# Optimization experiments

Hardware: AMD Instinct MI355X
Metric: run time of the kernel (lower is better)

Reference implementation:

```python
import jax, jax.numpy as jnp
import numpy as np

EPS_BN = 1e-5   # torch BatchNorm1d default eps
EPS_W = 1e-8    # inverse-distance weighting eps


def linear_bn_relu(x, W, b, gamma, beta, mean, var):
    # x: [B, N, Cin]; W: [Cout, Cin]. BatchNorm applied in eval mode with running stats.
    y = jnp.einsum('bnc,oc->bno', x, W) + b
    y = (y - mean) * (gamma / jnp.sqrt(var + EPS_BN)) + beta
    return jax.nn.relu(y)


def interpolate3(xyz_tgt, xyz_src, feats_src):
    # 3-NN inverse-distance-weighted interpolation (PointNetFeaturePropagation, mlp=[]).
    # xyz_tgt: [B,N,3], xyz_src: [B,S,3], feats_src: [B,S,C] -> [B,N,C]
    d = (jnp.sum(xyz_tgt * xyz_tgt, -1, keepdims=True)
         - 2.0 * jnp.einsum('bnd,bsd->bns', xyz_tgt, xyz_src)
         + jnp.sum(xyz_src * xyz_src, -1)[:, None, :])       # [B,N,S] squared dists
    neg_d, idx = jax.lax.top_k(-d, 3)                          # 3 smallest distances
    dists = -neg_d                                             # [B,N,3]
    w = 1.0 / (dists + EPS_W)
    w = w / jnp.sum(w, -1, keepdims=True)                      # [B,N,3]
    gathered = jax.vmap(lambda f, i: f[i])(feats_src, idx)     # [B,N,3,C]
    return jnp.sum(gathered * w[..., None], axis=2)            # [B,N,C]


def setup_inputs() -> dict:
    key = jax.random.key(0)
    ks = jax.random.split(key, 16)
    B, N1, N2 = 4, 4096, 16384
    dim1, dim2, dim_out = 512, 256, 256
    inp = {
        'xyz1': jax.random.normal(ks[0], (B, N1, 3), jnp.float32),
        'points1': jax.random.normal(ks[1], (B, N1, dim1), jnp.float32),
        'xyz2': jax.random.normal(ks[2], (B, N2, 3), jnp.float32),
        'points2': jax.random.normal(ks[3], (B, N2, dim2), jnp.float32),
        # fc1: Linear(dim1, dim_out) + BN(dim_out)
        'W1': jax.random.normal(ks[4], (dim_out, dim1), jnp.float32) * (dim1 ** -0.5),
        'b1': jax.random.normal(ks[5], (dim_out,), jnp.float32) * 0.01,
        'g1': jax.random.uniform(ks[6], (dim_out,), jnp.float32, 0.5, 1.5),
        'be1': jax.random.normal(ks[7], (dim_out,), jnp.float32) * 0.01,
        'm1': jax.random.normal(ks[8], (dim_out,), jnp.float32) * 0.01,
        'v1': jax.random.uniform(ks[9], (dim_out,), jnp.float32, 0.5, 1.5),
        # fc2: Linear(dim2, dim_out) + BN(dim_out)
        'W2': jax.random.normal(ks[10], (dim_out, dim2), jnp.float32) * (dim2 ** -0.5),
        'b2': jax.random.normal(ks[11], (dim_out,), jnp.float32) * 0.01,
        'g2': jax.random.uniform(ks[12], (dim_out,), jnp.float32, 0.5, 1.5),
        'be2': jax.random.normal(ks[13], (dim_out,), jnp.float32) * 0.01,
        'm2': jax.random.normal(ks[14], (dim_out,), jnp.float32) * 0.01,
        'v2': jax.random.uniform(ks[15], (dim_out,), jnp.float32, 0.5, 1.5),
    }
    return inp


def reference(xyz1, points1, xyz2, points2,
              W1, b1, g1, be1, m1, v1,
              W2, b2, g2, be2, m2, v2):
    feats1 = linear_bn_relu(points1, W1, b1, g1, be1, m1, v1)  # [B,N1,dim_out]
    feats2 = linear_bn_relu(points2, W2, b2, g2, be2, m2, v2)  # [B,N2,dim_out]
    interp = interpolate3(xyz2, xyz1, feats1)                  # [B,N2,dim_out]
    return interp + feats2
```

## Files before the change

kernel.cpp:

```cpp
#include <hip/hip_runtime.h>
#include <math.h>

#define EPS_BN 1e-5f

typedef __attribute__((ext_vector_type(8))) short bf16x8;
typedef __attribute__((ext_vector_type(4))) float f32x4;
typedef __attribute__((ext_vector_type(8))) _Float16 fp16x8;
typedef __attribute__((ext_vector_type(16))) float f32x16;

__device__ __forceinline__ void gld_lds16(const void* g, void* l) {
    __builtin_amdgcn_global_load_lds(
        (const __attribute__((address_space(1))) unsigned int*)g,
        (__attribute__((address_space(3))) unsigned int*)l, 16, 0, 0);
}

__device__ __forceinline__ unsigned short f2bf(float f) {
    unsigned u = __float_as_uint(f);
    return (unsigned short)((u + 0x7FFFu + ((u >> 16) & 1u)) >> 16);
}

__device__ __forceinline__ float dist_exact(float4 T, float4 s) {
    float dot2 = __fadd_rn(__fadd_rn(__fmul_rn(T.x, s.x), __fmul_rn(T.y, s.y)),
                           __fmul_rn(T.z, s.z));
    return __fadd_rn(__fsub_rn(T.w, dot2), s.w);
}

__device__ __forceinline__ float min3f(float a, float b, float c) {
    float d;
    asm("v_min3_f32 %0, %1, %2, %3" : "=v"(d) : "v"(a), "v"(b), "v"(c));
    return d;
}
__device__ __forceinline__ unsigned med3u(unsigned a, unsigned b, unsigned c) {
    unsigned d;
    asm("v_med3_u32 %0, %1, %2, %3" : "=v"(d) : "v"(a), "v"(b), "v"(c));
    return d;
}

__device__ __forceinline__ void conv_body(
    const float* __restrict__ src, unsigned short* __restrict__ dst,
    int blk, int tid, int K8log, int nslab)
{
    const int gid = blk * 256 + tid;
    const int m  = gid >> K8log;
    const int ko = gid & ((1 << K8log) - 1);
    const float4* s = (const float4*)src + ((size_t)m << (K8log + 1)) + ko * 2;
    float4 f0 = s[0];
    float4 f1 = s[1];
    const int mblk = m >> 7, r = m & 127;
    const int slab = ko >> 2, o = ko & 3;
    const int g = (o + (r >> 1)) & 3;
    unsigned short h[8] = {f2bf(f0.x), f2bf(f0.y), f2bf(f0.z), f2bf(f0.w),
                           f2bf(f1.x), f2bf(f1.y), f2bf(f1.z), f2bf(f1.w)};
    *(uint4*)(dst + ((size_t)(mblk * nslab + slab)) * 4096 + r * 32 + g * 8) =
        *(uint4*)h;
}

__global__ __launch_bounds__(256) void prep_all(
    const float* __restrict__ p1, const float* __restrict__ p2,
    const float* __restrict__ w1, const float* __restrict__ w2,
    unsigned short* __restrict__ A1p, unsigned short* __restrict__ A2p,
    unsigned short* __restrict__ W1p, unsigned short* __restrict__ W2p,
    const float* __restrict__ xyz1, const float* __restrict__ xyz2,
    float4* __restrict__ sxyz1, _Float16* __restrict__ srcpk,
    _Float16* __restrict__ tgtpk, float4* __restrict__ txyz2)
{
    const int blk = blockIdx.x, tid = threadIdx.x;
    if (blk < 4096)        conv_body(p1, A1p, blk,         tid, 6, 16);
    else if (blk < 12288)  conv_body(p2, A2p, blk - 4096,  tid, 5, 8);
    else if (blk < 12352)  conv_body(w1, W1p, blk - 12288, tid, 6, 16);
    else if (blk < 12384)  conv_body(w2, W2p, blk - 12352, tid, 5, 8);
    else if (blk < 12448) {
        int i = (blk - 12384) * 256 + tid;
        float x = xyz1[i * 3 + 0], y = xyz1[i * 3 + 1], z = xyz1[i * 3 + 2];
        float ss = __fadd_rn(__fadd_rn(__fmul_rn(x, x), __fmul_rn(y, y)),
                             __fmul_rn(z, z));
        float x2 = x + x, y2 = y + y, z2 = z + z;
        sxyz1[i] = make_float4(x2, y2, z2, ss);
        float nx = -x2, ny = -y2, nz = -z2;
        _Float16 hx = (_Float16)nx, lx = (_Float16)(nx - (float)hx);
        _Float16 hy = (_Float16)ny, ly = (_Float16)(ny - (float)hy);
        _Float16 hz = (_Float16)nz, lz = (_Float16)(nz - (float)hz);
        _Float16 hw = (_Float16)ss, lw = (_Float16)(ss - (float)hw);
        _Float16 z0 = (_Float16)0.f;
        fp16x8 lo8 = {hx, hx, lx, hy, hy, ly, hz, hz};
        fp16x8 hi8 = {lz, hw, lw, z0, z0, z0, z0, z0};
        *(fp16x8*)(srcpk + (size_t)i * 16)     = lo8;
        *(fp16x8*)(srcpk + (size_t)i * 16 + 8) = hi8;
    } else {
        int i = (blk - 12448) * 256 + tid;
        float x = xyz2[i * 3 + 0], y = xyz2[i * 3 + 1], z = xyz2[i * 3 + 2];
        float st = __fadd_rn(__fadd_rn(__fmul_rn(x, x), __fmul_rn(y, y)),
                             __fmul_rn(z, z));
        txyz2[i] = make_float4(x, y, z, st);
        _Float16 hx = (_Float16)x, lx = (_Float16)(x - (float)hx);
        _Float16 hy = (_Float16)y, ly = (_Float16)(y - (float)hy);
        _Float16 hz = (_Float16)z, lz = (_Float16)(z - (float)hz);
        _Float16 z0 = (_Float16)0.f, one = (_Float16)1.0f;
        fp16x8 lo8 = {hx, lx, hx, hy, ly, hy, hz, lz};
        fp16x8 hi8 = {hz, one, one, z0, z0, z0, z0, z0};
        *(fp16x8*)(tgtpk + (size_t)i * 16)     = lo8;
        *(fp16x8*)(tgtpk + (size_t)i * 16 + 8) = hi8;
    }
}

__global__ __launch_bounds__(256) void knn_mfma(
    const float4* __restrict__ sxyz1,
    const _Float16* __restrict__ srcpk,
    const _Float16* __restrict__ tgtpk,
    const float4* __restrict__ txyz2,
    float* __restrict__ w3, int* __restrict__ idx3)
{
    const int tid  = threadIdx.x;
    const int wv   = tid >> 6;
    const int lane = tid & 63;
    const int col  = lane & 31;
    const int h    = lane >> 5;
    const int tgt  = blockIdx.x * 128 + wv * 32 + col;
    const int batch = tgt >> 14;

    const float4 T = txyz2[tgt];
    const fp16x8 bfrag = *(const fp16x8*)(tgtpk + (size_t)tgt * 16 + h * 8);
    const _Float16* __restrict__ ap =
        srcpk + (size_t)batch * 4096 * 16 + (size_t)col * 16 + h * 8;
    const float4* __restrict__ S = sxyz1 + batch * 4096;

    const f32x16 zacc = {0.f,0.f,0.f,0.f, 0.f,0.f,0.f,0.f,
                         0.f,0.f,0.f,0.f, 0.f,0.f,0.f,0.f};

    unsigned k0 = 0xFFFFFFFFu, k1 = 0xFFFFFFFFu, k2 = 0xFFFFFFFFu,
             k3 = 0xFFFFFFFFu, k4 = 0xFFFFFFFFu, k5 = 0xFFFFFFFFu,
             k6 = 0xFFFFFFFFu, k7 = 0xFFFFFFFFu, k8 = 0xFFFFFFFFu,
             k9 = 0xFFFFFFFFu, k10 = 0xFFFFFFFFu, k11 = 0xFFFFFFFFu;

#pragma unroll 4
    for (int b = 0; b < 128; b++) {
        fp16x8 afrag = *(const fp16x8*)(ap + (size_t)b * 512);
        f32x16 acc = __builtin_amdgcn_mfma_f32_32x32x16_f16(
            afrag, bfrag, zacc, 0, 0, 0);
        float m1 = min3f(acc[0], acc[1], acc[2]);
        float m2 = min3f(acc[3], acc[4], acc[5]);
        float m3 = min3f(acc[6], acc[7], acc[8]);
        float m4 = min3f(acc[9], acc[10], acc[11]);
        float m5 = min3f(acc[12], acc[13], acc[14]);
        float m6 = min3f(m1, m2, m3);
        float m7 = min3f(m4, m5, acc[15]);
        float m  = fminf(m6, m7);

        int fu = __float_as_int(m);
        unsigned fk = (unsigned)(fu ^ ((fu >> 31) | 0x80000000));
        unsigned key = (fk & 0xFFFFFF80u) | (unsigned)b;

        unsigned nk0 = key < k0 ? key : k0;
        k11 = med3u(key, k10, k11);
        k10 = med3u(key, k9, k10);
        k9  = med3u(key, k8, k9);
        k8  = med3u(key, k7, k8);
        k7  = med3u(key, k6, k7);
        k6  = med3u(key, k5, k6);
        k5  = med3u(key, k4, k5);
        k4  = med3u(key, k3, k4);
        k3  = med3u(key, k2, k3);
        k2  = med3u(key, k1, k2);
        k1  = med3u(key, k0, k1);
        k0  = nk0;
    }

    const double INITK = __hiloint2double(0x7F800000, 0);
    double K0 = INITK, K1 = INITK, K2 = INITK;
#define INS3(kk) { if ((kk) < K2) {                                  \
        if ((kk) < K1) { K2 = K1;                                    \
            if ((kk) < K0) { K1 = K0; K0 = (kk); } else K1 = (kk);   \
        } else K2 = (kk); } }

#pragma unroll 1
    for (int r = 0; r < 12; r++) {
        const int bb = (int)(k0 & 127u);
        const float4* Sb = S + bb * 32 + 4 * h;
        const int sbase = bb * 32 + 4 * h;
#pragma unroll
        for (int e = 0; e < 16; e++) {
            const int row = (e & 3) + 8 * (e >> 2);
            float4 s = Sb[row];
            float d = dist_exact(T, s);
            double kk = __hiloint2double(__float_as_int(d), sbase + row);
            INS3(kk);
        }
        k0 = k1; k1 = k2; k2 = k3; k3 = k4; k4 = k5; k5 = k6;
        k6 = k7; k7 = k8; k8 = k9; k9 = k10; k10 = k11;
    }

    double O0 = __shfl_xor(K0, 32);
    double O1 = __shfl_xor(K1, 32);
    double O2 = __shfl_xor(K2, 32);
    INS3(O0); INS3(O1); INS3(O2);
#undef INS3

    if (h == 0) {
        float d0 = __int_as_float(__double2hiint(K0));
        float d1 = __int_as_float(__double2hiint(K1));
        float d2 = __int_as_float(__double2hiint(K2));
        float w0 = 1.0f / __fadd_rn(d0, 1e-8f);
        float w1 = 1.0f / __fadd_rn(d1, 1e-8f);
        float w2 = 1.0f / __fadd_rn(d2, 1e-8f);
        float ws = __fadd_rn(__fadd_rn(w0, w1), w2);
        w3[(size_t)tgt * 3 + 0] = w0 / ws;
        w3[(size_t)tgt * 3 + 1] = w1 / ws;
        w3[(size_t)tgt * 3 + 2] = w2 / ws;
        idx3[(size_t)tgt * 3 + 0] = __double2loint(K0);
        idx3[(size_t)tgt * 3 + 1] = __double2loint(K1);
        idx3[(size_t)tgt * 3 + 2] = __double2loint(K2);
    }
}

__global__ __launch_bounds__(256) void gemm_bf16_bn_relu(
    const unsigned short* __restrict__ Ap,
    const unsigned short* __restrict__ Bp,
    const float* __restrict__ bias,
    const float* __restrict__ gamma,
    const float* __restrict__ beta,
    const float* __restrict__ mean,
    const float* __restrict__ var,
    float* __restrict__ out, int M, int K)
{
    __shared__ __align__(16) unsigned short As[4096];
    __shared__ __align__(16) unsigned short Bs[4096];

    const int tid  = threadIdx.x;
    const int w    = tid >> 6;
    const int lane = tid & 63;
    const int q    = lane >> 4;
    const int rl   = lane & 15;
    const int wm   = w >> 1, wn = w & 1;
    const int bn   = blockIdx.x, bm = blockIdx.y;
    const int nslab = K >> 5;

    f32x4 acc[4][4];
#pragma unroll
    for (int i = 0; i < 4; i++)
#pragma unroll
        for (int j = 0; j < 4; j++) acc[i][j] = (f32x4){0.f, 0.f, 0.f, 0.f};

    const unsigned short* Ab = Ap + (size_t)bm * nslab * 4096;
    const unsigned short* Bb = Bp + (size_t)bn * nslab * 4096;
    const int c0 = 2 * w;
    const int l8 = lane * 8;

    int aidx[4], bidx[4];
#pragma unroll
    for (int i = 0; i < 4; i++) {
        int rr = wm * 64 + i * 16 + rl;
        aidx[i] = rr * 32 + ((q + (rr >> 1)) & 3) * 8;
        int nn = wn * 64 + i * 16 + rl;
        bidx[i] = nn * 32 + ((q + (nn >> 1)) & 3) * 8;
    }

    for (int s = 0; s < nslab; s++) {
        __syncthreads();
        const unsigned short* a = Ab + (size_t)s * 4096;
        const unsigned short* b = Bb + (size_t)s * 4096;
        gld_lds16(a + (c0 + 0) * 512 + l8, &As[(c0 + 0) * 512 + l8]);
        gld_lds16(a + (c0 + 1) * 512 + l8, &As[(c0 + 1) * 512 + l8]);
        gld_lds16(b + (c0 + 0) * 512 + l8, &Bs[(c0 + 0) * 512 + l8]);
        gld_lds16(b + (c0 + 1) * 512 + l8, &Bs[(c0 + 1) * 512 + l8]);
        __syncthreads();

        bf16x8 af[4], bf[4];
#pragma unroll
        for (int i = 0; i < 4; i++) af[i] = *(const bf16x8*)&As[aidx[i]];
#pragma unroll
        for (int j = 0; j < 4; j++) bf[j] = *(const bf16x8*)&Bs[bidx[j]];
#pragma unroll
        for (int i = 0; i < 4; i++)
#pragma unroll
            for (int j = 0; j < 4; j++)
                acc[i][j] = __builtin_amdgcn_mfma_f32_16x16x32_bf16(
                    af[i], bf[j], acc[i][j], 0, 0, 0);
    }

    const int gm0 = bm * 128 + wm * 64;
    const int gn0 = bn * 128 + wn * 64;
#pragma unroll
    for (int j = 0; j < 4; j++) {
        int n = gn0 + j * 16 + rl;
        float sc = gamma[n] / sqrtf(var[n] + EPS_BN);
        float sh = beta[n] + (bias[n] - mean[n]) * sc;
#pragma unroll
        for (int i = 0; i < 4; i++) {
            int m0 = gm0 + i * 16 + q * 4;
#pragma unroll
            for (int t = 0; t < 4; t++) {
                float v = fmaxf(acc[i][j][t] * sc + sh, 0.f);
                out[(size_t)(m0 + t) * 256 + n] = v;
            }
        }
    }
}

__global__ __launch_bounds__(256) void gemm2_interp(
    const unsigned short* __restrict__ Ap,
    const unsigned short* __restrict__ Bp,
    const float* __restrict__ bias,
    const float* __restrict__ gamma,
    const float* __restrict__ beta,
    const float* __restrict__ mean,
    const float* __restrict__ var,
    const float* __restrict__ feats1,
    const float* __restrict__ w3,
    const int*   __restrict__ idx3,
    float* __restrict__ out)
{
    __shared__ __align__(16) unsigned short As[4096];
    __shared__ __align__(16) unsigned short Bs[4096];

    const int tid  = threadIdx.x;
    const int w    = tid >> 6;
    const int lane = tid & 63;
    const int q    = lane >> 4;
    const int rl   = lane & 15;
    const int wm   = w >> 1, wn = w & 1;
    const int bn   = blockIdx.x, bm = blockIdx.y;
    const int nslab = 8;

    f32x4 acc[4][4];
#pragma unroll
    for (int i = 0; i < 4; i++)
#pragma unroll
        for (int j = 0; j < 4; j++) acc[i][j] = (f32x4){0.f, 0.f, 0.f, 0.f};

    const unsigned short* Ab = Ap + (size_t)bm * nslab * 4096;
    const unsigned short* Bb = Bp + (size_t)bn * nslab * 4096;
    const int c0 = 2 * w;
    const int l8 = lane * 8;

    int aidx[4], bidx[4];
#pragma unroll
    for (int i = 0; i < 4; i++) {
        int rr = wm * 64 + i * 16 + rl;
        aidx[i] = rr * 32 + ((q + (rr >> 1)) & 3) * 8;
        int nn = wn * 64 + i * 16 + rl;
        bidx[i] = nn * 32 + ((q + (nn >> 1)) & 3) * 8;
    }

    for (int s = 0; s < nslab; s++) {
        __syncthreads();
        const unsigned short* a = Ab + (size_t)s * 4096;
        const unsigned short* b = Bb + (size_t)s * 4096;
        gld_lds16(a + (c0 + 0) * 512 + l8, &As[(c0 + 0) * 512 + l8]);
        gld_lds16(a + (c0 + 1) * 512 + l8, &As[(c0 + 1) * 512 + l8]);
        gld_lds16(b + (c0 + 0) * 512 + l8, &Bs[(c0 + 0) * 512 + l8]);
        gld_lds16(b + (c0 + 1) * 512 + l8, &Bs[(c0 + 1) * 512 + l8]);
        __syncthreads();

        bf16x8 af[4], bf[4];
#pragma unroll
        for (int i = 0; i < 4; i++) af[i] = *(const bf16x8*)&As[aidx[i]];
#pragma unroll
        for (int j = 0; j < 4; j++) bf[j] = *(const bf16x8*)&Bs[bidx[j]];
#pragma unroll
        for (int i = 0; i < 4; i++)
#pragma unroll
            for (int j = 0; j < 4; j++)
                acc[i][j] = __builtin_amdgcn_mfma_f32_16x16x32_bf16(
                    af[i], bf[j], acc[i][j], 0, 0, 0);
    }

    const int gm0 = bm * 128 + wm * 64;
    const int gn0 = bn * 128 + wn * 64;
    float scj[4], shj[4];
    int nj[4];
#pragma unroll
    for (int j = 0; j < 4; j++) {
        int n = gn0 + j * 16 + rl;
        nj[j] = n;
        float sc = gamma[n] / sqrtf(var[n] + EPS_BN);
        scj[j] = sc;
        shj[j] = beta[n] + (bias[n] - mean[n]) * sc;
    }

#pragma unroll
    for (int i = 0; i < 4; i++) {
#pragma unroll
        for (int t = 0; t < 4; t++) {
            const int m = gm0 + i * 16 + q * 4 + t;
            const int bb = m >> 14;
            const int j0 = idx3[(size_t)m * 3 + 0];
            const int j1 = idx3[(size_t)m * 3 + 1];
            const int j2 = idx3[(size_t)m * 3 + 2];
            const float u0 = w3[(size_t)m * 3 + 0];
            const float u1 = w3[(size_t)m * 3 + 1];
            const float u2 = w3[(size_t)m * 3 + 2];
            const float* f0 = feats1 + ((size_t)(bb * 4096 + j0)) * 256;
            const float* f1 = feats1 + ((size_t)(bb * 4096 + j1)) * 256;
            const float* f2 = feats1 + ((size_t)(bb * 4096 + j2)) * 256;
#pragma unroll
            for (int j = 0; j < 4; j++) {
                const int n = nj[j];
                float v = fmaxf(acc[i][j][t] * scj[j] + shj[j], 0.f);
                v += u0 * f0[n] + u1 * f1[n] + u2 * f2[n];
                out[(size_t)m * 256 + n] = v;
            }
        }
    }
}

extern "C" void kernel_launch(void* const* d_in, const int* in_sizes, int n_in,
                              void* d_out, int out_size, void* d_ws, size_t ws_size,
                              hipStream_t stream) {
    const float* xyz1    = (const float*)d_in[0];
    const float* points1 = (const float*)d_in[1];
    const float* xyz2    = (const float*)d_in[2];
    const float* points2 = (const float*)d_in[3];
    const float* W1  = (const float*)d_in[4];
    const float* b1  = (const float*)d_in[5];
    const float* g1  = (const float*)d_in[6];
    const float* be1 = (const float*)d_in[7];
    const float* m1  = (const float*)d_in[8];
    const float* v1  = (const float*)d_in[9];
    const float* W2  = (const float*)d_in[10];
    const float* b2  = (const float*)d_in[11];
    const float* g2  = (const float*)d_in[12];
    const float* be2 = (const float*)d_in[13];
    const float* m2  = (const float*)d_in[14];
    const float* v2  = (const float*)d_in[15];

    const size_t MB = 1u << 20;
    char* ws = (char*)d_ws;
    float*          feats1 = (float*)(ws);
    _Float16*       srcpk  = (_Float16*)(ws);
    _Float16*       tgtpk  = (_Float16*)(ws + 1 * MB);
    unsigned short* A1p    = (unsigned short*)(ws + 16 * MB);
    unsigned short* A2p    = (unsigned short*)(ws + 32 * MB);
    unsigned short* W1p    = (unsigned short*)(ws + 64 * MB);
    unsigned short* W2p    = (unsigned short*)(ws + 64 * MB + 512 * 1024);
    float4*         sxyz1  = (float4*)(ws + 65 * MB);
    float4*         txyz2  = (float4*)(ws + 66 * MB);
    float*          w3     = (float*)(ws + 67 * MB);
    int*            idx3   = (int*)(ws + 68 * MB);
    float* outp = (float*)d_out;

    dim3 blk(256);
    prep_all<<<12704, blk, 0, stream>>>(points1, points2, W1, W2,
                                        A1p, A2p, W1p, W2p,
                                        xyz1, xyz2, sxyz1, srcpk, tgtpk, txyz2);
    knn_mfma<<<512, blk, 0, stream>>>(sxyz1, srcpk, tgtpk, txyz2, w3, idx3);
    gemm_bf16_bn_relu<<<dim3(2, 128), blk, 0, stream>>>(A1p, W1p, b1, g1, be1, m1, v1,
                                                        feats1, 16384, 512);
    gemm2_interp<<<dim3(2, 512), blk, 0, stream>>>(A2p, W2p, b2, g2, be2, m2, v2,
                                                   feats1, w3, idx3, outp);
}
```

Before: 317.3 us.

## Split KNN source scan into four partitions with a separate merge kernel

The KNN kernel now splits the 4096 source points of each batch into four partitions of 32 MFMA tiles each. It launches four times as many blocks, and each block writes its partial top-3 candidates (packed distance and index) to a workspace buffer. A new merge kernel reduces the 12 candidates per target and computes the inverse-distance weights. The A-fragment load is also software-prefetched one iteration ahead. This raises occupancy and parallelism on a grid that previously had only 512 blocks, at the cost of repeating the 12-round exact-distance refinement per partition, an extra kernel launch, and extra global traffic for the candidates.

```diff
diff --git a/kernel.cpp b/kernel.cpp
--- a/kernel.cpp
+++ b/kernel.cpp
@@ -103,25 +103,27 @@
     }
 }
 
-__global__ __launch_bounds__(256) void knn_mfma(
+__global__ __launch_bounds__(256) void knn_part(
     const float4* __restrict__ sxyz1,
     const _Float16* __restrict__ srcpk,
     const _Float16* __restrict__ tgtpk,
     const float4* __restrict__ txyz2,
-    float* __restrict__ w3, int* __restrict__ idx3)
+    double* __restrict__ cand)
 {
     const int tid  = threadIdx.x;
     const int wv   = tid >> 6;
     const int lane = tid & 63;
     const int col  = lane & 31;
     const int h    = lane >> 5;
-    const int tgt  = blockIdx.x * 128 + wv * 32 + col;
+    const int grp  = blockIdx.x & 511;
+    const int part = blockIdx.x >> 9;
+    const int tgt  = grp * 128 + wv * 32 + col;
     const int batch = tgt >> 14;
 
     const float4 T = txyz2[tgt];
     const fp16x8 bfrag = *(const fp16x8*)(tgtpk + (size_t)tgt * 16 + h * 8);
     const _Float16* __restrict__ ap =
-        srcpk + (size_t)batch * 4096 * 16 + (size_t)col * 16 + h * 8;
+        srcpk + (size_t)batch * 65536 + (size_t)col * 16 + h * 8;
     const float4* __restrict__ S = sxyz1 + batch * 4096;
 
     const f32x16 zacc = {0.f,0.f,0.f,0.f, 0.f,0.f,0.f,0.f,
@@ -132,11 +134,14 @@
              k6 = 0xFFFFFFFFu, k7 = 0xFFFFFFFFu, k8 = 0xFFFFFFFFu,
              k9 = 0xFFFFFFFFu, k10 = 0xFFFFFFFFu, k11 = 0xFFFFFFFFu;
 
+    const int b0 = part * 32;
+    fp16x8 af = *(const fp16x8*)(ap + (size_t)b0 * 512);
 #pragma unroll 4
-    for (int b = 0; b < 128; b++) {
-        fp16x8 afrag = *(const fp16x8*)(ap + (size_t)b * 512);
+    for (int b = b0; b < b0 + 32; b++) {
+        fp16x8 afn = af;
+        if (b < b0 + 31) afn = *(const fp16x8*)(ap + (size_t)(b + 1) * 512);
         f32x16 acc = __builtin_amdgcn_mfma_f32_32x32x16_f16(
-            afrag, bfrag, zacc, 0, 0, 0);
+            af, bfrag, zacc, 0, 0, 0);
         float m1 = min3f(acc[0], acc[1], acc[2]);
         float m2 = min3f(acc[3], acc[4], acc[5]);
         float m3 = min3f(acc[6], acc[7], acc[8]);
@@ -163,6 +168,7 @@
         k2  = med3u(key, k1, k2);
         k1  = med3u(key, k0, k1);
         k0  = nk0;
+        af = afn;
     }
 
     const double INITK = __hiloint2double(0x7F800000, 0);
@@ -196,20 +202,42 @@
 #undef INS3
 
     if (h == 0) {
-        float d0 = __int_as_float(__double2hiint(K0));
-        float d1 = __int_as_float(__double2hiint(K1));
-        float d2 = __int_as_float(__double2hiint(K2));
-        float w0 = 1.0f / __fadd_rn(d0, 1e-8f);
-        float w1 = 1.0f / __fadd_rn(d1, 1e-8f);
-        float w2 = 1.0f / __fadd_rn(d2, 1e-8f);
-        float ws = __fadd_rn(__fadd_rn(w0, w1), w2);
-        w3[(size_t)tgt * 3 + 0] = w0 / ws;
-        w3[(size_t)tgt * 3 + 1] = w1 / ws;
-        w3[(size_t)tgt * 3 + 2] = w2 / ws;
-        idx3[(size_t)tgt * 3 + 0] = __double2loint(K0);
-        idx3[(size_t)tgt * 3 + 1] = __double2loint(K1);
-        idx3[(size_t)tgt * 3 + 2] = __double2loint(K2);
-    }
+        double* c = cand + (size_t)tgt * 12 + part * 3;
+        c[0] = K0; c[1] = K1; c[2] = K2;
+    }
+}
+
+__global__ __launch_bounds__(256) void knn_merge(
+    const double* __restrict__ cand, float* __restrict__ w3,
+    int* __restrict__ idx3)
+{
+    const int g = blockIdx.x * 256 + threadIdx.x;
+    const double INIT = __hiloint2double(0x7F800000, 0);
+    double k0 = INIT, k1 = INIT, k2 = INIT;
+#pragma unroll
+    for (int p = 0; p < 12; p++) {
+        double k = cand[(size_t)g * 12 + p];
+        if (k < k2) {
+            if (k < k1) {
+                k2 = k1;
+                if (k < k0) { k1 = k0; k0 = k; }
+                else        { k1 = k; }
+            } else { k2 = k; }
+        }
+    }
+    float d0 = __int_as_float(__double2hiint(k0));
+    float d1 = __int_as_float(__double2hiint(k1));
+    float d2 = __int_as_float(__double2hiint(k2));
+    float w0 = 1.0f / __fadd_rn(d0, 1e-8f);
+    float w1 = 1.0f / __fadd_rn(d1, 1e-8f);
+    float w2 = 1.0f / __fadd_rn(d2, 1e-8f);
+    float ws = __fadd_rn(__fadd_rn(w0, w1), w2);
+    w3[(size_t)g * 3 + 0] = w0 / ws;
+    w3[(size_t)g * 3 + 1] = w1 / ws;
+    w3[(size_t)g * 3 + 2] = w2 / ws;
+    idx3[(size_t)g * 3 + 0] = __double2loint(k0);
+    idx3[(size_t)g * 3 + 1] = __double2loint(k1);
+    idx3[(size_t)g * 3 + 2] = __double2loint(k2);
 }
 
 __global__ __launch_bounds__(256) void gemm_bf16_bn_relu(
@@ -428,6 +456,7 @@
     float*          feats1 = (float*)(ws);
     _Float16*       srcpk  = (_Float16*)(ws);
     _Float16*       tgtpk  = (_Float16*)(ws + 1 * MB);
+    double*         cand   = (double*)(ws + 4 * MB);
     unsigned short* A1p    = (unsigned short*)(ws + 16 * MB);
     unsigned short* A2p    = (unsigned short*)(ws + 32 * MB);
     unsigned short* W1p    = (unsigned short*)(ws + 64 * MB);
@@ -442,7 +471,8 @@
     prep_all<<<12704, blk, 0, stream>>>(points1, points2, W1, W2,
                                         A1p, A2p, W1p, W2p,
                                         xyz1, xyz2, sxyz1, srcpk, tgtpk, txyz2);
-    knn_mfma<<<512, blk, 0, stream>>>(sxyz1, srcpk, tgtpk, txyz2, w3, idx3);
+    knn_part<<<2048, blk, 0, stream>>>(sxyz1, srcpk, tgtpk, txyz2, cand);
+    knn_merge<<<256, blk, 0, stream>>>(cand, w3, idx3);
     gemm_bf16_bn_relu<<<dim3(2, 128), blk, 0, stream>>>(A1p, W1p, b1, g1, be1, m1, v1,
                                                         feats1, 16384, 512);
     gemm2_interp<<<dim3(2, 512), blk, 0, stream>>>(A2p, W2p, b2, g2, be2, m2, v2,
```

Measured after the change: 406.2 us. +28.0%, slower.

## Split KNN source scan across four waves per target group with LDS merge

Applied to the files above, without the earlier changes.

The KNN kernel now has each block handle 32 targets instead of 128. Its four waves each scan a quarter of the 128 source blocks. The per-wave top-12 block keys are merged through LDS, each wave refines three of the merged candidates exactly, and a final LDS reduction picks the top three. This shortens the serial 128-step chain per thread and launches four times as many blocks, adding a software prefetch of the next A fragment. The cost is two barriers, an extra 48-key insertion pass, and more LDS use per block.

```diff
diff --git a/kernel.cpp b/kernel.cpp
--- a/kernel.cpp
+++ b/kernel.cpp
@@ -103,25 +103,29 @@
     }
 }
 
-__global__ __launch_bounds__(256) void knn_mfma(
+__global__ __launch_bounds__(256) void knn_fused(
     const float4* __restrict__ sxyz1,
     const _Float16* __restrict__ srcpk,
     const _Float16* __restrict__ tgtpk,
     const float4* __restrict__ txyz2,
     float* __restrict__ w3, int* __restrict__ idx3)
 {
+    __shared__ unsigned keys_lds[64 * 49];
+    __shared__ double   tails_lds[32 * 13];
+
     const int tid  = threadIdx.x;
     const int wv   = tid >> 6;
     const int lane = tid & 63;
     const int col  = lane & 31;
     const int h    = lane >> 5;
-    const int tgt  = blockIdx.x * 128 + wv * 32 + col;
+    const int tgtg = blockIdx.x;
+    const int tgt  = tgtg * 32 + col;
     const int batch = tgt >> 14;
 
     const float4 T = txyz2[tgt];
     const fp16x8 bfrag = *(const fp16x8*)(tgtpk + (size_t)tgt * 16 + h * 8);
     const _Float16* __restrict__ ap =
-        srcpk + (size_t)batch * 4096 * 16 + (size_t)col * 16 + h * 8;
+        srcpk + (size_t)batch * 65536 + (size_t)col * 16 + h * 8;
     const float4* __restrict__ S = sxyz1 + batch * 4096;
 
     const f32x16 zacc = {0.f,0.f,0.f,0.f, 0.f,0.f,0.f,0.f,
@@ -132,11 +136,14 @@
              k6 = 0xFFFFFFFFu, k7 = 0xFFFFFFFFu, k8 = 0xFFFFFFFFu,
              k9 = 0xFFFFFFFFu, k10 = 0xFFFFFFFFu, k11 = 0xFFFFFFFFu;
 
+    const int b0 = wv * 32;
+    fp16x8 af = *(const fp16x8*)(ap + (size_t)b0 * 512);
 #pragma unroll 4
-    for (int b = 0; b < 128; b++) {
-        fp16x8 afrag = *(const fp16x8*)(ap + (size_t)b * 512);
+    for (int b = b0; b < b0 + 32; b++) {
+        fp16x8 afn = af;
+        if (b < b0 + 31) afn = *(const fp16x8*)(ap + (size_t)(b + 1) * 512);
         f32x16 acc = __builtin_amdgcn_mfma_f32_32x32x16_f16(
-            afrag, bfrag, zacc, 0, 0, 0);
+            af, bfrag, zacc, 0, 0, 0);
         float m1 = min3f(acc[0], acc[1], acc[2]);
         float m2 = min3f(acc[3], acc[4], acc[5]);
         float m3 = min3f(acc[6], acc[7], acc[8]);
@@ -163,7 +170,50 @@
         k2  = med3u(key, k1, k2);
         k1  = med3u(key, k0, k1);
         k0  = nk0;
-    }
+        af = afn;
+    }
+
+    {
+        unsigned* kw = &keys_lds[(h * 32 + col) * 49 + wv * 12];
+        kw[0] = k0;  kw[1] = k1;  kw[2] = k2;  kw[3] = k3;
+        kw[4] = k4;  kw[5] = k5;  kw[6] = k6;  kw[7] = k7;
+        kw[8] = k8;  kw[9] = k9;  kw[10] = k10; kw[11] = k11;
+    }
+    __syncthreads();
+
+    unsigned s0 = 0xFFFFFFFFu, s1 = 0xFFFFFFFFu, s2 = 0xFFFFFFFFu,
+             s3 = 0xFFFFFFFFu, s4 = 0xFFFFFFFFu, s5 = 0xFFFFFFFFu,
+             s6 = 0xFFFFFFFFu, s7 = 0xFFFFFFFFu, s8 = 0xFFFFFFFFu,
+             s9 = 0xFFFFFFFFu, s10 = 0xFFFFFFFFu, s11 = 0xFFFFFFFFu;
+#define INSK(key) {                                                   \
+        unsigned n0 = (key) < s0 ? (key) : s0;                        \
+        s11 = med3u((key), s10, s11);                                 \
+        s10 = med3u((key), s9, s10);                                  \
+        s9  = med3u((key), s8, s9);                                   \
+        s8  = med3u((key), s7, s8);                                   \
+        s7  = med3u((key), s6, s7);                                   \
+        s6  = med3u((key), s5, s6);                                   \
+        s5  = med3u((key), s4, s5);                                   \
+        s4  = med3u((key), s3, s4);                                   \
+        s3  = med3u((key), s2, s3);                                   \
+        s2  = med3u((key), s1, s2);                                   \
+        s1  = med3u((key), s0, s1);                                   \
+        s0  = n0; }
+    {
+        const unsigned* kr = &keys_lds[(h * 32 + col) * 49];
+#pragma unroll 8
+        for (int c = 0; c < 48; c++) {
+            unsigned key = kr[c];
+            INSK(key);
+        }
+    }
+#undef INSK
+
+    unsigned r0, r1, r2;
+    if      (wv == 0) { r0 = s0; r1 = s1;  r2 = s2;  }
+    else if (wv == 1) { r0 = s3; r1 = s4;  r2 = s5;  }
+    else if (wv == 2) { r0 = s6; r1 = s7;  r2 = s8;  }
+    else              { r0 = s9; r1 = s10; r2 = s11; }
 
     const double INITK = __hiloint2double(0x7F800000, 0);
     double K0 = INITK, K1 = INITK, K2 = INITK;
@@ -172,9 +222,10 @@
             if ((kk) < K0) { K1 = K0; K0 = (kk); } else K1 = (kk);   \
         } else K2 = (kk); } }
 
-#pragma unroll 1
-    for (int r = 0; r < 12; r++) {
-        const int bb = (int)(k0 & 127u);
+#pragma unroll
+    for (int r = 0; r < 3; r++) {
+        const unsigned rr = (r == 0) ? r0 : ((r == 1) ? r1 : r2);
+        const int bb = (int)(rr & 127u);
         const float4* Sb = S + bb * 32 + 4 * h;
         const int sbase = bb * 32 + 4 * h;
 #pragma unroll
@@ -185,8 +236,6 @@
             double kk = __hiloint2double(__float_as_int(d), sbase + row);
             INS3(kk);
         }
-        k0 = k1; k1 = k2; k2 = k3; k3 = k4; k4 = k5; k5 = k6;
-        k6 = k7; k7 = k8; k8 = k9; k9 = k10; k10 = k11;
     }
 
     double O0 = __shfl_xor(K0, 32);
@@ -196,19 +245,37 @@
 #undef INS3
 
     if (h == 0) {
-        float d0 = __int_as_float(__double2hiint(K0));
-        float d1 = __int_as_float(__double2hiint(K1));
-        float d2 = __int_as_float(__double2hiint(K2));
+        double* tw = &tails_lds[col * 13 + wv * 3];
+        tw[0] = K0; tw[1] = K1; tw[2] = K2;
+    }
+    __syncthreads();
+
+    if (tid < 32) {
+        double M0 = INITK, M1 = INITK, M2 = INITK;
+#define INSM(kk) { if ((kk) < M2) {                                  \
+        if ((kk) < M1) { M2 = M1;                                    \
+            if ((kk) < M0) { M1 = M0; M0 = (kk); } else M1 = (kk);   \
+        } else M2 = (kk); } }
+#pragma unroll
+        for (int p = 0; p < 12; p++) {
+            double kk = tails_lds[tid * 13 + p];
+            INSM(kk);
+        }
+#undef INSM
+        const int t = tgtg * 32 + tid;
+        float d0 = __int_as_float(__double2hiint(M0));
+        float d1 = __int_as_float(__double2hiint(M1));
+        float d2 = __int_as_float(__double2hiint(M2));
         float w0 = 1.0f / __fadd_rn(d0, 1e-8f);
         float w1 = 1.0f / __fadd_rn(d1, 1e-8f);
         float w2 = 1.0f / __fadd_rn(d2, 1e-8f);
         float ws = __fadd_rn(__fadd_rn(w0, w1), w2);
-        w3[(size_t)tgt * 3 + 0] = w0 / ws;
-        w3[(size_t)tgt * 3 + 1] = w1 / ws;
-        w3[(size_t)tgt * 3 + 2] = w2 / ws;
-        idx3[(size_t)tgt * 3 + 0] = __double2loint(K0);
-        idx3[(size_t)tgt * 3 + 1] = __double2loint(K1);
-        idx3[(size_t)tgt * 3 + 2] = __double2loint(K2);
+        w3[(size_t)t * 3 + 0] = w0 / ws;
+        w3[(size_t)t * 3 + 1] = w1 / ws;
+        w3[(size_t)t * 3 + 2] = w2 / ws;
+        idx3[(size_t)t * 3 + 0] = __double2loint(M0);
+        idx3[(size_t)t * 3 + 1] = __double2loint(M1);
+        idx3[(size_t)t * 3 + 2] = __double2loint(M2);
     }
 }
 
@@ -442,7 +509,7 @@
     prep_all<<<12704, blk, 0, stream>>>(points1, points2, W1, W2,
                                         A1p, A2p, W1p, W2p,
                                         xyz1, xyz2, sxyz1, srcpk, tgtpk, txyz2);
-    knn_mfma<<<512, blk, 0, stream>>>(sxyz1, srcpk, tgtpk, txyz2, w3, idx3);
+    knn_fused<<<2048, blk, 0, stream>>>(sxyz1, srcpk, tgtpk, txyz2, w3, idx3);
     gemm_bf16_bn_relu<<<dim3(2, 128), blk, 0, stream>>>(A1p, W1p, b1, g1, be1, m1, v1,
                                                         feats1, 16384, 512);
     gemm2_interp<<<dim3(2, 512), blk, 0, stream>>>(A2p, W2p, b2, g2, be2, m2, v2,
```

New measurement: 297.0 us. -6.4%, faster.
